# Kernel tuning notes

Measured on AMD Instinct MI355X. Metric: run time of the kernel, lower is better.

## Reference

```python
import jax, jax.numpy as jnp
import numpy as np

B, DIM = 4096, 768
HEADS, DIM_HEAD = 8, 96
INNER = HEADS * DIM_HEAD  # 768
N_IDS = 751


def setup_inputs() -> dict:
    key = jax.random.key(0)
    k1, k2, k3, k4 = jax.random.split(key, 4)
    x = jax.random.normal(k1, (B, DIM), dtype=jnp.float32)
    labels = jax.random.randint(k2, (B,), 0, N_IDS, dtype=jnp.int64)
    W_qkv = jax.random.normal(k3, (DIM, 3 * INNER), dtype=jnp.float32) * 0.02
    W_out = jax.random.normal(k4, (INNER, DIM), dtype=jnp.float32) * 0.02
    return {"x": x, "labels": labels, "W_qkv": W_qkv, "W_out": W_out}


def reference(x, labels, W_qkv, W_out):
    scale = DIM_HEAD ** -0.5
    qkv = x @ W_qkv  # [b, 3*inner]
    q, k, v = jnp.split(qkv, 3, axis=-1)  # each [b, inner]
    # rearrange 'b (h d) -> h b d'
    split_heads = lambda t: t.reshape(B, HEADS, DIM_HEAD).transpose(1, 0, 2)
    q, k, v = split_heads(q), split_heads(k), split_heads(v)
    dots = jnp.einsum('hid,hjd->hij', q, k) * scale  # [h, b, b]
    attn = jax.nn.softmax(dots, axis=-1)
    # post-softmax pairwise label-equality mask (no renormalization)
    mask = (labels[:, None] == labels[None, :]).astype(attn.dtype)  # [b, b]
    out = jnp.einsum('hij,hjd->hid', attn * mask[None], v)  # [h, b, d]
    out = out.transpose(1, 0, 2).reshape(B, INNER)  # 'h i d -> i (h d)'
    return out @ W_out
```

## Files before the change

kernel.cpp:

```cpp
#include <hip/hip_runtime.h>
#include <hip/hip_bf16.h>

#define BB 4096
#define DIMM 768
#define NHEADS 8
#define DHEAD 96
#define NIDS 751
#define QKSCALE 0.10206207261596577f
#define PVCH 96

typedef _Float16 f16x8 __attribute__((ext_vector_type(8)));
typedef float f32x4 __attribute__((ext_vector_type(4)));

__device__ __forceinline__ void split2(float v, _Float16* hi, _Float16* lo) {
    _Float16 h = (_Float16)v;
    *hi = h;
    *lo = (_Float16)(v - (float)h);
}

__device__ __forceinline__ float rec2(const _Float16* hi, const _Float16* lo, size_t idx) {
    return (float)hi[idx] + (float)lo[idx];
}

__device__ __forceinline__ void gl_lds16(const void* g, void* l) {
    __builtin_amdgcn_global_load_lds(
        (const __attribute__((address_space(1))) unsigned int*)g,
        (__attribute__((address_space(3))) unsigned int*)l, 16, 0, 0);
}

__global__ void k_zero(float* p, int n) {
    int i = blockIdx.x * blockDim.x + threadIdx.x;
    if (i < n) p[i] = 0.0f;
}

__global__ void k_split(const float* __restrict__ in, _Float16* __restrict__ hi,
                        _Float16* __restrict__ lo, float s, int n) {
    int i = blockIdx.x * blockDim.x + threadIdx.x;
    if (i < n) split2(in[i] * s, &hi[i], &lo[i]);
}

__global__ void k_tsplit(const float* __restrict__ W, _Float16* __restrict__ Th,
                         _Float16* __restrict__ Tl, float s, int K, int N) {
    __shared__ float tile[32][33];
    int k0 = blockIdx.y * 32, n0 = blockIdx.x * 32;
    int tx = threadIdx.x, ty = threadIdx.y;
    for (int r = ty; r < 32; r += 8) tile[r][tx] = W[(size_t)(k0 + r) * N + n0 + tx];
    __syncthreads();
    for (int r = ty; r < 32; r += 8) {
        int n = n0 + r, k = k0 + tx;
        split2(tile[tx][r] * s, &Th[(size_t)n * K + k], &Tl[(size_t)n * K + k]);
    }
}

__global__ __launch_bounds__(1024) void k_groups(
    const int* __restrict__ labels, int* __restrict__ perm,
    int* __restrict__ gstart, int* __restrict__ gcnt) {
    __shared__ int cnt[1024], scn[1024], strt[1024], cur[1024];
    int tid = threadIdx.x;
    cnt[tid] = 0; cur[tid] = 0;
    __syncthreads();
    for (int i = tid; i < BB; i += 1024) atomicAdd(&cnt[labels[i]], 1);
    __syncthreads();
    int v = cnt[tid];
    scn[tid] = v;
    __syncthreads();
#pragma unroll
    for (int off = 1; off < 1024; off <<= 1) {
        int t = (tid >= off) ? scn[tid - off] : 0;
        __syncthreads();
        scn[tid] += t;
        __syncthreads();
    }
    int st = scn[tid] - v;
    strt[tid] = st;
    if (tid < NIDS) { gstart[tid] = st; gcnt[tid] = v; }
    __syncthreads();
    for (int i = tid; i < BB; i += 1024) {
        int lb = labels[i];
        int p = strt[lb] + atomicAdd(&cur[lb], 1);
        perm[p] = i;
    }
}

template <int EPI>
__global__ __launch_bounds__(256) void k_gemm(
    const _Float16* __restrict__ Ah, const _Float16* __restrict__ Al, int lda,
    const _Float16* __restrict__ Bh, const _Float16* __restrict__ Bl, int ldb,
    int K, float inv,
    float* __restrict__ outF, _Float16* __restrict__ oh, _Float16* __restrict__ ol) {
    __shared__ __align__(16) _Float16 sAh[2][128 * 32];
    __shared__ __align__(16) _Float16 sAl[2][128 * 32];
    __shared__ __align__(16) _Float16 sBh[2][128 * 32];
    __shared__ __align__(16) _Float16 sBl[2][128 * 32];
    const int tid = threadIdx.x;
    const int lane = tid & 63;
    const int wave = tid >> 6;
    const int wm = wave >> 1, wn = wave & 1;
    unsigned wg = blockIdx.y * gridDim.x + blockIdx.x;
    unsigned nwg = gridDim.x * gridDim.y;
    unsigned swz = ((nwg & 7u) == 0u) ? (wg & 7u) * (nwg >> 3) + (wg >> 3) : wg;
    unsigned by = swz / gridDim.x;
    unsigned bx = swz - by * gridDim.x;
    const int m0 = by * 128, n0 = bx * 128;
    const int srow = tid >> 2;
    const int scol = (tid & 3) * 8;
    const int rl = lane & 15;
    const int g8 = (lane >> 4) * 8;

    const _Float16* gAh0 = Ah + (size_t)(m0 + srow) * lda + scol;
    const _Float16* gAh1 = gAh0 + (size_t)64 * lda;
    const _Float16* gAl0 = Al + (size_t)(m0 + srow) * lda + scol;
    const _Float16* gAl1 = gAl0 + (size_t)64 * lda;
    const _Float16* gBh0 = Bh + (size_t)(n0 + srow) * ldb + scol;
    const _Float16* gBh1 = gBh0 + (size_t)64 * ldb;
    const _Float16* gBl0 = Bl + (size_t)(n0 + srow) * ldb + scol;
    const _Float16* gBl1 = gBl0 + (size_t)64 * ldb;
    const int d0 = tid * 8, d1 = 2048 + tid * 8;

    auto stage = [&](int b, int kk) {
        gl_lds16(gAh0 + kk, &sAh[b][d0]);
        gl_lds16(gAh1 + kk, &sAh[b][d1]);
        gl_lds16(gAl0 + kk, &sAl[b][d0]);
        gl_lds16(gAl1 + kk, &sAl[b][d1]);
        gl_lds16(gBh0 + kk, &sBh[b][d0]);
        gl_lds16(gBh1 + kk, &sBh[b][d1]);
        gl_lds16(gBl0 + kk, &sBl[b][d0]);
        gl_lds16(gBl1 + kk, &sBl[b][d1]);
    };

    f32x4 acc[4][4];
    const f32x4 vzero = {0.f, 0.f, 0.f, 0.f};
#pragma unroll
    for (int a = 0; a < 4; a++)
#pragma unroll
        for (int b = 0; b < 4; b++) acc[a][b] = vzero;

    const int KS = K >> 5;
    stage(0, 0);
    for (int ks = 0; ks < KS; ks++) {
        __syncthreads();
        if (ks + 1 < KS) stage((ks + 1) & 1, (ks + 1) << 5);
        const int cb = ks & 1;
        f16x8 ah[4], al[4], bh[4], bl[4];
#pragma unroll
        for (int t = 0; t < 4; t++) {
            ah[t] = *(const f16x8*)&sAh[cb][(wm * 64 + t * 16 + rl) * 32 + g8];
            al[t] = *(const f16x8*)&sAl[cb][(wm * 64 + t * 16 + rl) * 32 + g8];
            bh[t] = *(const f16x8*)&sBh[cb][(wn * 64 + t * 16 + rl) * 32 + g8];
            bl[t] = *(const f16x8*)&sBl[cb][(wn * 64 + t * 16 + rl) * 32 + g8];
        }
#pragma unroll
        for (int a = 0; a < 4; a++)
#pragma unroll
            for (int b = 0; b < 4; b++) {
                acc[a][b] = __builtin_amdgcn_mfma_f32_16x16x32_f16(ah[a], bh[b], acc[a][b], 0, 0, 0);
                acc[a][b] = __builtin_amdgcn_mfma_f32_16x16x32_f16(ah[a], bl[b], acc[a][b], 0, 0, 0);
                acc[a][b] = __builtin_amdgcn_mfma_f32_16x16x32_f16(al[a], bh[b], acc[a][b], 0, 0, 0);
            }
    }

#pragma unroll
    for (int a = 0; a < 4; a++)
#pragma unroll
        for (int b = 0; b < 4; b++) {
            f32x4 d = acc[a][b] * inv;
            int n = n0 + wn * 64 + b * 16 + rl;
            int mb = m0 + wm * 64 + a * 16 + (lane >> 4) * 4;
#pragma unroll
            for (int r = 0; r < 4; r++) {
                int m = mb + r;
                if constexpr (EPI == 0) {
                    if (n < 1536) {
                        split2(d[r] * 16.0f, &oh[(size_t)m * 1536 + n], &ol[(size_t)m * 1536 + n]);
                    } else {
                        outF[(size_t)m * DIMM + (n - 1536)] = d[r];
                    }
                } else {
                    outF[(size_t)m * DIMM + n] = d[r];
                }
            }
        }
}

__global__ __launch_bounds__(256) void k_qksum(
    const _Float16* __restrict__ QKh, float* __restrict__ lsum) {
    __shared__ __align__(16) _Float16 sB[2][128 * 104];
    const int tid = threadIdx.x;
    const int lane = tid & 63;
    const int wave = tid >> 6;
    const int wm = wave >> 1, wn = wave & 1;
    unsigned wg = blockIdx.y * gridDim.x + blockIdx.x;
    const int head = (int)(wg & 7u);
    unsigned rest = wg >> 3;
    const int m0 = (int)(rest & 31u) * 128;
    const int nq = (int)(rest >> 5);
    const int cA = head * DHEAD;
    const int cB = DIMM + head * DHEAD;
    const int rl = lane & 15;
    const int g8 = (lane >> 4) * 8;

    f16x8 ah[3][4];
#pragma unroll
    for (int k = 0; k < 3; k++)
#pragma unroll
        for (int a = 0; a < 4; a++)
            ah[k][a] = *(const f16x8*)(QKh +
                (size_t)(m0 + wm * 64 + a * 16 + rl) * 1536 + cA + k * 32 + g8);

    auto stage = [&](int b, int tile) {
        const int n0 = tile * 128;
#pragma unroll
        for (int rd = 0; rd < 7; rd++) {
            int idx = rd * 256 + tid;
            if (idx < 1664) {
                int row = idx / 13;
                int c = idx - row * 13;
                int col = (c < 12) ? c * 8 : 0;
                gl_lds16(QKh + (size_t)(n0 + row) * 1536 + cB + col,
                         &sB[b][idx * 8]);
            }
        }
    };

    const f32x4 vzero = {0.f, 0.f, 0.f, 0.f};
    f32x4 es[4];
#pragma unroll
    for (int a = 0; a < 4; a++) es[a] = vzero;
    const float esc = QKSCALE * (1.0f / 256.0f);

    stage(0, nq * 8);
    for (int nt = 0; nt < 8; nt++) {
        __syncthreads();
        if (nt < 7) stage((nt + 1) & 1, nq * 8 + nt + 1);
        const int cb = nt & 1;
        f32x4 acc[4][4];
#pragma unroll
        for (int a = 0; a < 4; a++)
#pragma unroll
            for (int b = 0; b < 4; b++) acc[a][b] = vzero;
#pragma unroll
        for (int k = 0; k < 3; k++) {
            f16x8 bh[4];
#pragma unroll
            for (int b = 0; b < 4; b++)
                bh[b] = *(const f16x8*)&sB[cb][(wn * 64 + b * 16 + rl) * 104 + k * 32 + g8];
#pragma unroll
            for (int a = 0; a < 4; a++)
#pragma unroll
                for (int b = 0; b < 4; b++)
                    acc[a][b] = __builtin_amdgcn_mfma_f32_16x16x32_f16(ah[k][a], bh[b], acc[a][b], 0, 0, 0);
        }
#pragma unroll
        for (int a = 0; a < 4; a++)
#pragma unroll
            for (int b = 0; b < 4; b++)
#pragma unroll
                for (int r = 0; r < 4; r++)
                    es[a][r] += __expf(acc[a][b][r] * esc);
    }

    float (*red)[33] = (float (*)[33])&sB[0][0];
#pragma unroll
    for (int a = 0; a < 4; a++) {
        int rb = wm * 64 + a * 16 + (lane >> 4) * 4;
#pragma unroll
        for (int r = 0; r < 4; r++) red[rb + r][wn * 16 + rl] = es[a][r];
    }
    __syncthreads();
    if (tid < 128) {
        float s = 0.f;
#pragma unroll
        for (int c = 0; c < 32; c++) s += red[tid][c];
        atomicAdd(&lsum[(size_t)head * BB + m0 + tid], s);
    }
}

__global__ __launch_bounds__(768) void k_pv(
    const _Float16* __restrict__ QKh, const _Float16* __restrict__ QKl,
    const float* __restrict__ vbuf, const float* __restrict__ lsum,
    const int* __restrict__ labels, const int* __restrict__ perm,
    const int* __restrict__ gstart, const int* __restrict__ gcnt,
    _Float16* __restrict__ oh, _Float16* __restrict__ ol) {
    const int i = blockIdx.x;
    const int tid = threadIdx.x;
    const int wave = tid >> 6;
    const int lane = tid & 63;
    __shared__ float wv[NHEADS][PVCH];
    __shared__ int pidx[PVCH];
    const int lab = labels[i];
    const int st = gstart[lab];
    const int cnt = gcnt[lab];

    float q0 = 0.f, q1 = 0.f, invl = 0.f;
    if (wave < NHEADS) {
        size_t base = (size_t)i * 1536 + wave * DHEAD;
        q0 = rec2(QKh, QKl, base + lane);
        if (lane < 32) q1 = rec2(QKh, QKl, base + 64 + lane);
        invl = 1.0f / lsum[(size_t)wave * BB + i];
    }
    const int h = tid / DHEAD;
    float acc = 0.f;
    for (int b0 = 0; b0 < cnt; b0 += PVCH) {
        int ch = cnt - b0; if (ch > PVCH) ch = PVCH;
        __syncthreads();
        if (tid < ch) pidx[tid] = perm[st + b0 + tid];
        __syncthreads();
        if (wave < NHEADS) {
            for (int jj = 0; jj < ch; jj++) {
                size_t kb = (size_t)pidx[jj] * 1536 + DIMM + wave * DHEAD;
                float p = q0 * rec2(QKh, QKl, kb + lane);
                if (lane < 32) p += q1 * rec2(QKh, QKl, kb + 64 + lane);
#pragma unroll
                for (int m = 32; m >= 1; m >>= 1) p += __shfl_xor(p, m);
                if (lane == 0)
                    wv[wave][jj] = __expf(p * (1.0f / 256.0f) * QKSCALE) * invl;
            }
        }
        __syncthreads();
        for (int jj = 0; jj < ch; jj++)
            acc += wv[h][jj] * vbuf[(size_t)pidx[jj] * DIMM + tid];
    }
    split2(acc * 16.0f, &oh[(size_t)i * DIMM + tid], &ol[(size_t)i * DIMM + tid]);
}

extern "C" void kernel_launch(void* const* d_in, const int* in_sizes, int n_in,
                              void* d_out, int out_size, void* d_ws, size_t ws_size,
                              hipStream_t stream) {
    const float* x = (const float*)d_in[0];
    const int* labels = (const int*)d_in[1];
    const float* Wqkv = (const float*)d_in[2];
    const float* Wout = (const float*)d_in[3];
    float* out = (float*)d_out;

    char* ws = (char*)d_ws;
    size_t off = 0;
    auto alloc = [&](size_t bytes) -> void* {
        void* p = ws + off;
        off += (bytes + 255) & ~(size_t)255;
        return p;
    };
    _Float16* Xh   = (_Float16*)alloc((size_t)BB * DIMM * 2);
    _Float16* Xl   = (_Float16*)alloc((size_t)BB * DIMM * 2);
    _Float16* WqTh = (_Float16*)alloc((size_t)2304 * DIMM * 2);
    _Float16* WqTl = (_Float16*)alloc((size_t)2304 * DIMM * 2);
    _Float16* WoTh = (_Float16*)alloc((size_t)DIMM * DIMM * 2);
    _Float16* WoTl = (_Float16*)alloc((size_t)DIMM * DIMM * 2);
    _Float16* QKh  = (_Float16*)alloc((size_t)BB * 1536 * 2);
    _Float16* QKl  = (_Float16*)alloc((size_t)BB * 1536 * 2);
    float* vbuf    = (float*)alloc((size_t)BB * DIMM * 4);
    float* lsum    = (float*)alloc((size_t)NHEADS * BB * 4);
    _Float16* Oh   = (_Float16*)alloc((size_t)BB * DIMM * 2);
    _Float16* Ol   = (_Float16*)alloc((size_t)BB * DIMM * 2);
    int* perm      = (int*)alloc(BB * 4);
    int* gstart    = (int*)alloc(1024 * 4);
    int* gcnt      = (int*)alloc(1024 * 4);

    k_zero<<<dim3((NHEADS * BB + 255) / 256), dim3(256), 0, stream>>>(lsum, NHEADS * BB);
    k_split<<<dim3((BB * DIMM + 255) / 256), dim3(256), 0, stream>>>(x, Xh, Xl, 16.0f, BB * DIMM);
    k_tsplit<<<dim3(2304 / 32, DIMM / 32), dim3(32, 8), 0, stream>>>(Wqkv, WqTh, WqTl, 256.0f, DIMM, 2304);
    k_tsplit<<<dim3(DIMM / 32, DIMM / 32), dim3(32, 8), 0, stream>>>(Wout, WoTh, WoTl, 256.0f, DIMM, DIMM);
    k_groups<<<dim3(1), dim3(1024), 0, stream>>>(labels, perm, gstart, gcnt);

    k_gemm<0><<<dim3(2304 / 128, BB / 128, 1), dim3(256), 0, stream>>>(
        Xh, Xl, DIMM, WqTh, WqTl, DIMM, DIMM, 1.0f / 4096.0f, vbuf, QKh, QKl);
    k_qksum<<<dim3(32, 32), dim3(256), 0, stream>>>(QKh, lsum);
    k_pv<<<dim3(BB), dim3(768), 0, stream>>>(QKh, QKl, vbuf, lsum, labels, perm, gstart, gcnt, Oh, Ol);
    k_gemm<1><<<dim3(DIMM / 128, BB / 128, 1), dim3(256), 0, stream>>>(
        Oh, Ol, DIMM, WoTh, WoTl, DIMM, DIMM, 1.0f / 4096.0f, out, nullptr, nullptr);
}
```

Measured before the change: 303.8 us.

## Use 8-wave GEMM tiles, split-K output projection, and 256-thread PV blocks

The GEMM kernel now runs 512 threads (8 waves) per 128x128 tile, each wave owning a 64x32 sub-tile, which lowers accumulator registers and raises occupancy. The output projection is split along K into two z-slices that accumulate into the output with atomicAdd, so the output must be zeroed first by a fused zero kernel. The PV kernel drops from 768 to 256 threads, with each thread handling three output columns and waves looping over every head for the score computation. The atomics add nondeterminism and contention, and the smaller PV blocks change how the work is spread across the GPU.

```diff
diff --git a/kernel.cpp b/kernel.cpp
--- a/kernel.cpp
+++ b/kernel.cpp
@@ -28,9 +28,11 @@
         (__attribute__((address_space(3))) unsigned int*)l, 16, 0, 0);
 }
 
-__global__ void k_zero(float* p, int n) {
+__global__ void k_zero2(float* a, int na, float* b, int nb) {
     int i = blockIdx.x * blockDim.x + threadIdx.x;
-    if (i < n) p[i] = 0.0f;
+    if (i < na) a[i] = 0.0f;
+    int j = i - na;
+    if (j >= 0 && j < nb) b[j] = 0.0f;
 }
 
 __global__ void k_split(const float* __restrict__ in, _Float16* __restrict__ hi,
@@ -83,7 +85,7 @@
 }
 
 template <int EPI>
-__global__ __launch_bounds__(256) void k_gemm(
+__global__ __launch_bounds__(512, 4) void k_gemm(
     const _Float16* __restrict__ Ah, const _Float16* __restrict__ Al, int lda,
     const _Float16* __restrict__ Bh, const _Float16* __restrict__ Bl, int ldb,
     int K, float inv,
@@ -95,45 +97,38 @@
     const int tid = threadIdx.x;
     const int lane = tid & 63;
     const int wave = tid >> 6;
-    const int wm = wave >> 1, wn = wave & 1;
+    const int wm = wave >> 2, wn = wave & 3;
     unsigned wg = blockIdx.y * gridDim.x + blockIdx.x;
     unsigned nwg = gridDim.x * gridDim.y;
     unsigned swz = ((nwg & 7u) == 0u) ? (wg & 7u) * (nwg >> 3) + (wg >> 3) : wg;
     unsigned by = swz / gridDim.x;
     unsigned bx = swz - by * gridDim.x;
     const int m0 = by * 128, n0 = bx * 128;
+    const int kbase = blockIdx.z * K;
     const int srow = tid >> 2;
     const int scol = (tid & 3) * 8;
     const int rl = lane & 15;
     const int g8 = (lane >> 4) * 8;
 
-    const _Float16* gAh0 = Ah + (size_t)(m0 + srow) * lda + scol;
-    const _Float16* gAh1 = gAh0 + (size_t)64 * lda;
-    const _Float16* gAl0 = Al + (size_t)(m0 + srow) * lda + scol;
-    const _Float16* gAl1 = gAl0 + (size_t)64 * lda;
-    const _Float16* gBh0 = Bh + (size_t)(n0 + srow) * ldb + scol;
-    const _Float16* gBh1 = gBh0 + (size_t)64 * ldb;
-    const _Float16* gBl0 = Bl + (size_t)(n0 + srow) * ldb + scol;
-    const _Float16* gBl1 = gBl0 + (size_t)64 * ldb;
-    const int d0 = tid * 8, d1 = 2048 + tid * 8;
+    const _Float16* gAh0 = Ah + (size_t)(m0 + srow) * lda + kbase + scol;
+    const _Float16* gAl0 = Al + (size_t)(m0 + srow) * lda + kbase + scol;
+    const _Float16* gBh0 = Bh + (size_t)(n0 + srow) * ldb + kbase + scol;
+    const _Float16* gBl0 = Bl + (size_t)(n0 + srow) * ldb + kbase + scol;
+    const int d0 = tid * 8;
 
     auto stage = [&](int b, int kk) {
         gl_lds16(gAh0 + kk, &sAh[b][d0]);
-        gl_lds16(gAh1 + kk, &sAh[b][d1]);
         gl_lds16(gAl0 + kk, &sAl[b][d0]);
-        gl_lds16(gAl1 + kk, &sAl[b][d1]);
         gl_lds16(gBh0 + kk, &sBh[b][d0]);
-        gl_lds16(gBh1 + kk, &sBh[b][d1]);
         gl_lds16(gBl0 + kk, &sBl[b][d0]);
-        gl_lds16(gBl1 + kk, &sBl[b][d1]);
     };
 
-    f32x4 acc[4][4];
+    f32x4 acc[4][2];
     const f32x4 vzero = {0.f, 0.f, 0.f, 0.f};
 #pragma unroll
     for (int a = 0; a < 4; a++)
 #pragma unroll
-        for (int b = 0; b < 4; b++) acc[a][b] = vzero;
+        for (int b = 0; b < 2; b++) acc[a][b] = vzero;
 
     const int KS = K >> 5;
     stage(0, 0);
@@ -141,18 +136,21 @@
         __syncthreads();
         if (ks + 1 < KS) stage((ks + 1) & 1, (ks + 1) << 5);
         const int cb = ks & 1;
-        f16x8 ah[4], al[4], bh[4], bl[4];
+        f16x8 ah[4], al[4], bh[2], bl[2];
 #pragma unroll
         for (int t = 0; t < 4; t++) {
             ah[t] = *(const f16x8*)&sAh[cb][(wm * 64 + t * 16 + rl) * 32 + g8];
             al[t] = *(const f16x8*)&sAl[cb][(wm * 64 + t * 16 + rl) * 32 + g8];
-            bh[t] = *(const f16x8*)&sBh[cb][(wn * 64 + t * 16 + rl) * 32 + g8];
-            bl[t] = *(const f16x8*)&sBl[cb][(wn * 64 + t * 16 + rl) * 32 + g8];
+        }
+#pragma unroll
+        for (int u = 0; u < 2; u++) {
+            bh[u] = *(const f16x8*)&sBh[cb][(wn * 32 + u * 16 + rl) * 32 + g8];
+            bl[u] = *(const f16x8*)&sBl[cb][(wn * 32 + u * 16 + rl) * 32 + g8];
         }
 #pragma unroll
         for (int a = 0; a < 4; a++)
 #pragma unroll
-            for (int b = 0; b < 4; b++) {
+            for (int b = 0; b < 2; b++) {
                 acc[a][b] = __builtin_amdgcn_mfma_f32_16x16x32_f16(ah[a], bh[b], acc[a][b], 0, 0, 0);
                 acc[a][b] = __builtin_amdgcn_mfma_f32_16x16x32_f16(ah[a], bl[b], acc[a][b], 0, 0, 0);
                 acc[a][b] = __builtin_amdgcn_mfma_f32_16x16x32_f16(al[a], bh[b], acc[a][b], 0, 0, 0);
@@ -162,9 +160,9 @@
 #pragma unroll
     for (int a = 0; a < 4; a++)
 #pragma unroll
-        for (int b = 0; b < 4; b++) {
+        for (int b = 0; b < 2; b++) {
             f32x4 d = acc[a][b] * inv;
-            int n = n0 + wn * 64 + b * 16 + rl;
+            int n = n0 + wn * 32 + b * 16 + rl;
             int mb = m0 + wm * 64 + a * 16 + (lane >> 4) * 4;
 #pragma unroll
             for (int r = 0; r < 4; r++) {
@@ -176,7 +174,7 @@
                         outF[(size_t)m * DIMM + (n - 1536)] = d[r];
                     }
                 } else {
-                    outF[(size_t)m * DIMM + n] = d[r];
+                    atomicAdd(&outF[(size_t)m * DIMM + n], d[r]);
                 }
             }
         }
@@ -275,7 +273,7 @@
     }
 }
 
-__global__ __launch_bounds__(768) void k_pv(
+__global__ __launch_bounds__(256) void k_pv(
     const _Float16* __restrict__ QKh, const _Float16* __restrict__ QKl,
     const float* __restrict__ vbuf, const float* __restrict__ lsum,
     const int* __restrict__ labels, const int* __restrict__ perm,
@@ -290,37 +288,46 @@
     const int lab = labels[i];
     const int st = gstart[lab];
     const int cnt = gcnt[lab];
-
-    float q0 = 0.f, q1 = 0.f, invl = 0.f;
-    if (wave < NHEADS) {
-        size_t base = (size_t)i * 1536 + wave * DHEAD;
-        q0 = rec2(QKh, QKl, base + lane);
-        if (lane < 32) q1 = rec2(QKh, QKl, base + 64 + lane);
-        invl = 1.0f / lsum[(size_t)wave * BB + i];
-    }
-    const int h = tid / DHEAD;
-    float acc = 0.f;
+    const float esc = QKSCALE * (1.0f / 256.0f);
+
+    float q0[NHEADS], q1[NHEADS], invl[NHEADS];
+#pragma unroll
+    for (int h = 0; h < NHEADS; h++) {
+        size_t base = (size_t)i * 1536 + h * DHEAD;
+        q0[h] = rec2(QKh, QKl, base + lane);
+        q1[h] = (lane < 32) ? rec2(QKh, QKl, base + 64 + lane) : 0.0f;
+        invl[h] = 1.0f / lsum[(size_t)h * BB + i];
+    }
+    const int d1 = tid + 256, d2 = tid + 512;
+    const int h0 = tid / DHEAD, h1 = d1 / DHEAD, h2 = d2 / DHEAD;
+    float acc0 = 0.f, acc1 = 0.f, acc2 = 0.f;
+
     for (int b0 = 0; b0 < cnt; b0 += PVCH) {
         int ch = cnt - b0; if (ch > PVCH) ch = PVCH;
         __syncthreads();
         if (tid < ch) pidx[tid] = perm[st + b0 + tid];
         __syncthreads();
-        if (wave < NHEADS) {
-            for (int jj = 0; jj < ch; jj++) {
-                size_t kb = (size_t)pidx[jj] * 1536 + DIMM + wave * DHEAD;
-                float p = q0 * rec2(QKh, QKl, kb + lane);
-                if (lane < 32) p += q1 * rec2(QKh, QKl, kb + 64 + lane);
-#pragma unroll
-                for (int m = 32; m >= 1; m >>= 1) p += __shfl_xor(p, m);
-                if (lane == 0)
-                    wv[wave][jj] = __expf(p * (1.0f / 256.0f) * QKSCALE) * invl;
-            }
-        }
-        __syncthreads();
-        for (int jj = 0; jj < ch; jj++)
-            acc += wv[h][jj] * vbuf[(size_t)pidx[jj] * DIMM + tid];
-    }
-    split2(acc * 16.0f, &oh[(size_t)i * DIMM + tid], &ol[(size_t)i * DIMM + tid]);
+        for (int t = wave; t < NHEADS * ch; t += 4) {
+            int hh = t & 7, jj = t >> 3;
+            size_t kb = (size_t)pidx[jj] * 1536 + DIMM + hh * DHEAD;
+            float p = q0[hh] * rec2(QKh, QKl, kb + lane);
+            if (lane < 32) p += q1[hh] * rec2(QKh, QKl, kb + 64 + lane);
+#pragma unroll
+            for (int m = 32; m >= 1; m >>= 1) p += __shfl_xor(p, m);
+            if (lane == 0) wv[hh][jj] = __expf(p * esc) * invl[hh];
+        }
+        __syncthreads();
+        for (int jj = 0; jj < ch; jj++) {
+            const float* vr = vbuf + (size_t)pidx[jj] * DIMM;
+            acc0 += wv[h0][jj] * vr[tid];
+            acc1 += wv[h1][jj] * vr[d1];
+            acc2 += wv[h2][jj] * vr[d2];
+        }
+    }
+    size_t ob = (size_t)i * DIMM;
+    split2(acc0 * 16.0f, &oh[ob + tid], &ol[ob + tid]);
+    split2(acc1 * 16.0f, &oh[ob + d1], &ol[ob + d1]);
+    split2(acc2 * 16.0f, &oh[ob + d2], &ol[ob + d2]);
 }
 
 extern "C" void kernel_launch(void* const* d_in, const int* in_sizes, int n_in,
@@ -355,16 +362,17 @@
     int* gstart    = (int*)alloc(1024 * 4);
     int* gcnt      = (int*)alloc(1024 * 4);
 
-    k_zero<<<dim3((NHEADS * BB + 255) / 256), dim3(256), 0, stream>>>(lsum, NHEADS * BB);
+    const int nz = NHEADS * BB + BB * DIMM;
+    k_zero2<<<dim3((nz + 255) / 256), dim3(256), 0, stream>>>(lsum, NHEADS * BB, out, BB * DIMM);
     k_split<<<dim3((BB * DIMM + 255) / 256), dim3(256), 0, stream>>>(x, Xh, Xl, 16.0f, BB * DIMM);
     k_tsplit<<<dim3(2304 / 32, DIMM / 32), dim3(32, 8), 0, stream>>>(Wqkv, WqTh, WqTl, 256.0f, DIMM, 2304);
     k_tsplit<<<dim3(DIMM / 32, DIMM / 32), dim3(32, 8), 0, stream>>>(Wout, WoTh, WoTl, 256.0f, DIMM, DIMM);
     k_groups<<<dim3(1), dim3(1024), 0, stream>>>(labels, perm, gstart, gcnt);
 
-    k_gemm<0><<<dim3(2304 / 128, BB / 128, 1), dim3(256), 0, stream>>>(
+    k_gemm<0><<<dim3(2304 / 128, BB / 128, 1), dim3(512), 0, stream>>>(
         Xh, Xl, DIMM, WqTh, WqTl, DIMM, DIMM, 1.0f / 4096.0f, vbuf, QKh, QKl);
     k_qksum<<<dim3(32, 32), dim3(256), 0, stream>>>(QKh, lsum);
-    k_pv<<<dim3(BB), dim3(768), 0, stream>>>(QKh, QKl, vbuf, lsum, labels, perm, gstart, gcnt, Oh, Ol);
-    k_gemm<1><<<dim3(DIMM / 128, BB / 128, 1), dim3(256), 0, stream>>>(
-        Oh, Ol, DIMM, WoTh, WoTl, DIMM, DIMM, 1.0f / 4096.0f, out, nullptr, nullptr);
-}
+    k_pv<<<dim3(BB), dim3(256), 0, stream>>>(QKh, QKl, vbuf, lsum, labels, perm, gstart, gcnt, Oh, Ol);
+    k_gemm<1><<<dim3(DIMM / 128, BB / 128, 2), dim3(512), 0, stream>>>(
+        Oh, Ol, DIMM, WoTh, WoTl, DIMM, 384, 1.0f / 4096.0f, out, nullptr, nullptr);
+}
```

New measurement: 312.3 us. +2.8%, slower.
